# Optimization experiments

Hardware: AMD Instinct MI355X
Metric: run time of the kernel (lower is better)

## Reference

```python
import jax, jax.numpy as jnp
import numpy as np
from jax.scipy.special import logsumexp

N, M, D = 4096, 4096, 512
MASS = 0.9
REG = 0.1
REG_KL = 0.01
ITERS = 100


def setup_inputs() -> dict:
    key = jax.random.key(0)
    k0, k1 = jax.random.split(key)
    return {
        "ft0": jax.random.normal(k0, (N, D), dtype=jnp.float32),
        "ft1": jax.random.normal(k1, (M, D), dtype=jnp.float32),
        "bin_score": jnp.float32(0.4),
    }


def reference(ft0, ft1, bin_score):
    # all rows have norm >> 1e-8 for randn inputs -> foreground masks are all True
    f0 = ft0 / jnp.linalg.norm(ft0, axis=-1, keepdims=True)
    f1 = ft1 / jnp.linalg.norm(ft1, axis=-1, keepdims=True)
    cos_sim = f0 @ f1.T                       # [N, M]
    n, m = cos_sim.shape

    # partial OT marginals with dustbin mass (get_partial_distributions)
    a = jnp.concatenate([jnp.full((n,), MASS / n, jnp.float32),
                         jnp.array([1.0 - MASS], jnp.float32)])
    b = jnp.concatenate([jnp.full((m,), MASS / m, jnp.float32),
                         jnp.array([1.0 - MASS], jnp.float32)])
    log_mu, log_nu = jnp.log(a), jnp.log(b)   # [n+1], [m+1]

    # augment score matrix with dustbin row/col (get_partial_ot_problem)
    top = jnp.concatenate([cos_sim, jnp.broadcast_to(bin_score, (n, 1))], axis=1)
    bot = jnp.broadcast_to(bin_score, (1, m + 1))
    couplings = jnp.concatenate([top, bot], axis=0)   # [n+1, m+1]

    lmba = 1.0 / REG                         # = 10.0
    phi = REG_KL / (REG_KL + 1.0 / lmba)     # = 0.01 / 0.11
    Z = lmba * couplings

    def body(carry, _):
        u, v = carry
        u = (log_mu - logsumexp(Z + v[None, :] * lmba, axis=1)) / lmba * phi
        v = (log_nu - logsumexp(Z + u[:, None] * lmba, axis=0)) / lmba * phi
        return (u, v), None

    u0 = jnp.zeros((n + 1,), jnp.float32)
    v0 = jnp.zeros((m + 1,), jnp.float32)
    (u, v), _ = jax.lax.scan(body, (u0, v0), None, length=ITERS)

    prob = jnp.exp(Z + u[:, None] * lmba + v[None, :] * lmba)
    # prob_add_bkg with all-True masks: identity placement, zero the corner
    return prob.at[-1, -1].set(0.0)
```

## Files before the change

### kernel.cpp

```cpp
#include <hip/hip_runtime.h>
#include <math.h>

#define Nn 4096
#define Mm 4096
#define Dd 512
#define NP 4097
#define NPB 4104

#define PHI 0.09090909090909091f
#define LMU_IN  (-8.4231266823771690f)
#define LMU_BIN (-2.3025850929940457f)
#define LOG_NP  8.3180489582454150f

typedef __attribute__((ext_vector_type(8))) __bf16 bf16x8;
typedef __attribute__((ext_vector_type(4))) float  f32x4;

__device__ __forceinline__ void load_lds16(const __bf16* g, __bf16* l) {
    __builtin_amdgcn_global_load_lds(
        (__attribute__((address_space(1))) void*)g,
        (__attribute__((address_space(3))) void*)l,
        16, 0, 0);
}

__device__ __forceinline__ float block_allreduce_256(float v, float* sb) {
    #pragma unroll
    for (int off = 32; off > 0; off >>= 1) v += __shfl_down(v, off, 64);
    __syncthreads();
    if ((threadIdx.x & 63) == 0) sb[threadIdx.x >> 6] = v;
    __syncthreads();
    return sb[0] + sb[1] + sb[2] + sb[3];
}

__global__ __launch_bounds__(256) void normalize_bins_kernel(
    const float* __restrict__ F0, const float* __restrict__ F1,
    const float* __restrict__ binp,
    __bf16* __restrict__ A, __bf16* __restrict__ B, _Float16* __restrict__ Ef,
    float* __restrict__ S0, float* __restrict__ TcA) {
    __shared__ float sb[4];
    const int row = blockIdx.x;
    const float* src = (row < Nn) ? (F0 + (size_t)row * Dd)
                                  : (F1 + (size_t)(row - Nn) * Dd);
    __bf16* dst = (row < Nn) ? (A + (size_t)row * Dd)
                             : (B + (size_t)(row - Nn) * Dd);
    const float2 x = ((const float2*)src)[threadIdx.x];
    const float s = block_allreduce_256(x.x * x.x + x.y * x.y, sb);
    const float rn = rsqrtf(s);
    dst[2 * threadIdx.x]     = (__bf16)(x.x * rn);
    dst[2 * threadIdx.x + 1] = (__bf16)(x.y * rn);

    if (row < 17) {
        const int j = row * 256 + threadIdx.x;
        if (j < NP) Ef[(size_t)Nn * NPB + j] = (_Float16)__expf(10.0f * binp[0]);
    } else if (row < 33) {
        const int i = (row - 17) * 256 + threadIdx.x;
        Ef[(size_t)i * NPB + Mm] = (_Float16)__expf(10.0f * binp[0]);
    } else if (row < 50) {
        const int k = (row - 33) * 256 + threadIdx.x;
        if (k < NP) S0[k] = 0.f;
    } else if (row < 67) {
        const int k = (row - 50) * 256 + threadIdx.x;
        if (k < NP) TcA[k] = 0.f;
    }
}

#define BKh 32
__global__ __launch_bounds__(512, 2) void gemm_rowsum_kernel(
    const __bf16* __restrict__ A, const __bf16* __restrict__ B,
    _Float16* __restrict__ Ef, float* __restrict__ S0) {
    __shared__ __align__(16) __bf16 As[2][2][256 * BKh];
    __shared__ __align__(16) __bf16 Bs[2][2][256 * BKh];
    const int tid = threadIdx.x;
    const int l = tid & 63, wv = tid >> 6;
    const int wm = wv >> 2, wn = wv & 3;
    const int ln = l & 15, lq = l >> 4;

    const int bid = blockIdx.x;
    const int xcd = bid & 7, sub = bid >> 3;
    const int by = (xcd & 3) * 4 + (sub >> 3);
    const int bx = (xcd >> 2) * 8 + (sub & 7);
    const int row0 = by << 8, col0 = bx << 8;

    f32x4 acc[8][4];
    #pragma unroll
    for (int i = 0; i < 8; ++i)
        #pragma unroll
        for (int j = 0; j < 4; ++j) acc[i][j] = (f32x4){0.f, 0.f, 0.f, 0.f};

    size_t aG[2], bG[2]; int qE[2];
    #pragma unroll
    for (int p = 0; p < 2; ++p) {
        const int q = tid + p * 512;
        const int r = q >> 2, c = q & 3;
        const int cg = c ^ ((r >> 1) & 3);
        aG[p] = (size_t)(row0 + r) * Dd + cg * 8;
        bG[p] = (size_t)(col0 + r) * Dd + cg * 8;
        qE[p] = q * 8;
    }

    auto STAGE_UNIT = [&](int nb, int tt, int u) {
        const size_t kofs = (size_t)(tt * 64 + (u >> 1) * 32);
        if ((u & 1) == 0) {
            load_lds16(A + aG[0] + kofs, &As[nb][u >> 1][qE[0]]);
            load_lds16(A + aG[1] + kofs, &As[nb][u >> 1][qE[1]]);
        } else {
            load_lds16(B + bG[0] + kofs, &Bs[nb][u >> 1][qE[0]]);
            load_lds16(B + bG[1] + kofs, &Bs[nb][u >> 1][qE[1]]);
        }
    };

    #define WAITV(N) asm volatile("s_waitcnt vmcnt(" #N ")" ::: "memory")
    #define BAR() __builtin_amdgcn_s_barrier()

    const int swz2 = (ln >> 1) & 3;

    STAGE_UNIT(0, 0, 0); STAGE_UNIT(0, 0, 1);
    STAGE_UNIT(0, 0, 2); STAGE_UNIT(0, 0, 3);
    WAITV(4); BAR();

    #pragma unroll
    for (int t = 0; t < 8; ++t) {
        const int buf = t & 1, nbuf = buf ^ 1;
        #pragma unroll
        for (int ks = 0; ks < 2; ++ks) {
            bf16x8 bfr[4];
            #pragma unroll
            for (int half = 0; half < 2; ++half) {
                const int p = ks * 2 + half;
                if (half == 0) {
                    #pragma unroll
                    for (int ni = 0; ni < 4; ++ni) {
                        const int r = wn * 64 + ni * 16 + ln;
                        bfr[ni] = *(const bf16x8*)
                            &Bs[buf][ks][r * BKh + ((lq ^ swz2) * 8)];
                    }
                }
                bf16x8 af[4];
                #pragma unroll
                for (int i = 0; i < 4; ++i) {
                    const int r = wm * 128 + half * 64 + i * 16 + ln;
                    af[i] = *(const bf16x8*)
                        &As[buf][ks][r * BKh + ((lq ^ swz2) * 8)];
                }
                if (t < 7) STAGE_UNIT(nbuf, t + 1, p);
                if (t < 7 || p == 0) { WAITV(4); }
                else if (p == 1)     { WAITV(0); }
                BAR();
                __builtin_amdgcn_s_setprio(1);
                #pragma unroll
                for (int i = 0; i < 4; ++i)
                    #pragma unroll
                    for (int ni = 0; ni < 4; ++ni)
                        acc[half * 4 + i][ni] =
                            __builtin_amdgcn_mfma_f32_16x16x32_bf16(
                                af[i], bfr[ni], acc[half * 4 + i][ni], 0, 0, 0);
                __builtin_amdgcn_s_setprio(0);
                BAR();
            }
        }
    }
    #undef WAITV
    #undef BAR

    #pragma unroll
    for (int mi = 0; mi < 8; ++mi) {
        #pragma unroll
        for (int r = 0; r < 4; ++r) {
            const int gi = row0 + wm * 128 + mi * 16 + lq * 4 + r;
            _Float16* bRow = Ef + (size_t)gi * NPB + col0 + wn * 64 + ln;
            float rs = 0.f;
            #pragma unroll
            for (int ni = 0; ni < 4; ++ni) {
                const float e = __expf(10.0f * acc[mi][ni][r]);
                bRow[ni * 16] = (_Float16)e;
                rs += e;
            }
            rs += __shfl_down(rs, 8, 64);
            rs += __shfl_down(rs, 4, 64);
            rs += __shfl_down(rs, 2, 64);
            rs += __shfl_down(rs, 1, 64);
            if (ln == 0) atomicAdd(&S0[gi], rs);
        }
    }
}

__global__ __launch_bounds__(256) void col_pass_kernel(
    const _Float16* __restrict__ Ef, const float* __restrict__ S0,
    const float* __restrict__ eUarr, const float* __restrict__ binp,
    float* __restrict__ Tc, const int mode) {
    __shared__ float evl[32];
    const int tid = threadIdx.x;
    const int t = blockIdx.x;
    const int sI = blockIdx.y;
    const int r0 = sI * 32;

    if (tid < 32) {
        const int r = r0 + tid;
        float ev;
        if (mode == 0) {
            const float ebin = __expf(10.0f * binp[0]);
            ev = __expf(PHI * (LMU_IN - __logf(S0[r] + ebin)));
        } else {
            ev = eUarr[r];
        }
        evl[tid] = ev;
    }
    __syncthreads();

    const int j0 = t * 512 + tid * 2;
    const unsigned short* base = (const unsigned short*)Ef;
    float s0 = 0.f, s1 = 0.f;
    #pragma unroll
    for (int k = 0; k < 32; ++k) {
        const int r = r0 + k;
        union { unsigned u; _Float16 h[2]; } e;
        e.u = *(const unsigned*)(base + (size_t)r * NPB + j0);
        const float ev = evl[k];
        s0 += (float)e.h[0] * ev;
        s1 += (float)e.h[1] * ev;
    }

    float ev4096 = 0.f;
    if (sI == 127) {
        ev4096 = (mode == 0)
               ? __expf(PHI * (LMU_BIN - (LOG_NP + 10.0f * binp[0])))
               : eUarr[Nn];
        union { unsigned u; _Float16 h[2]; } e;
        e.u = *(const unsigned*)(base + (size_t)Nn * NPB + j0);
        s0 += (float)e.h[0] * ev4096;
        s1 += (float)e.h[1] * ev4096;
    }
    atomicAdd(&Tc[j0], s0);
    atomicAdd(&Tc[j0 + 1], s1);

    if (t == 0 && tid < 64) {
        float sc = 0.f;
        if (tid < 32)
            sc = (float)Ef[(size_t)(r0 + tid) * NPB + Mm] * evl[tid];
        else if (tid == 32 && sI == 127)
            sc = (float)Ef[(size_t)Nn * NPB + Mm] * ev4096;
        #pragma unroll
        for (int off = 32; off > 0; off >>= 1) sc += __shfl_down(sc, off, 64);
        if (tid == 0) atomicAdd(&Tc[Mm], sc);
    }
}

__global__ __launch_bounds__(256) void row_pass2_kernel(
    const _Float16* __restrict__ Ef, const float* __restrict__ TcA,
    float* __restrict__ eU, float* __restrict__ TcB) {
    __shared__ float sb[4];
    __shared__ float wl[NP];
    const int tid = threadIdx.x;

    for (int j = tid; j < NP; j += 256) {
        const float lnu = (j < Mm) ? LMU_IN : LMU_BIN;
        wl[j] = __expf(PHI * (lnu - __logf(TcA[j])));
    }
    __syncthreads();

    const int i0 = blockIdx.x * 8;
    #pragma unroll 1
    for (int k = 0; k < 8; ++k) {
        const int i = i0 + k;
        if (i >= NP) break;
        const uint4* rowp = (const uint4*)(Ef + (size_t)i * NPB);
        float s = 0.f;
        #pragma unroll
        for (int c = 0; c < 2; ++c) {
            const int chunk = c * 256 + tid;
            union { uint4 u; _Float16 h[8]; } e;
            e.u = rowp[chunk];
            const float4 w0 = *(const float4*)&wl[chunk * 8];
            const float4 w1 = *(const float4*)&wl[chunk * 8 + 4];
            s += (float)e.h[0] * w0.x + (float)e.h[1] * w0.y
               + (float)e.h[2] * w0.z + (float)e.h[3] * w0.w
               + (float)e.h[4] * w1.x + (float)e.h[5] * w1.y
               + (float)e.h[6] * w1.z + (float)e.h[7] * w1.w;
        }
        if (tid == 0) s += (float)Ef[(size_t)i * NPB + Mm] * wl[Mm];
        s = block_allreduce_256(s, sb);
        if (tid == 0) {
            const float lmu = (i < Nn) ? LMU_IN : LMU_BIN;
            eU[i] = __expf(PHI * (lmu - __logf(s)));
        }
    }
    if (tid < 8 && i0 + tid < NP) TcB[i0 + tid] = 0.f;
}

__global__ __launch_bounds__(256) void finish_kernel(
    const _Float16* __restrict__ Ef, const float* __restrict__ eU,
    const float* __restrict__ TcB, float* __restrict__ out) {
    __shared__ float wl[NP];
    const int tid = threadIdx.x;
    for (int j = tid; j < NP; j += 256) {
        const float lnu = (j < Mm) ? LMU_IN : LMU_BIN;
        wl[j] = __expf(PHI * (lnu - __logf(TcB[j])));
    }
    __syncthreads();

    const int i0 = blockIdx.x * 8;
    #pragma unroll 1
    for (int k = 0; k < 8; ++k) {
        const int i = i0 + k;
        if (i >= NP) break;
        const float sU = eU[i];
        const unsigned* erow32 = (const unsigned*)(Ef + (size_t)i * NPB);
        float* orow = out + (size_t)i * NP;
        #pragma unroll
        for (int c = 0; c < 8; ++c) {
            const int j0 = c * 512 + tid * 2;
            union { unsigned u; _Float16 h[2]; } e;
            e.u = erow32[c * 256 + tid];
            const float2 wv = *(const float2*)&wl[j0];
            orow[j0]     = (float)e.h[0] * sU * wv.x;
            orow[j0 + 1] = (float)e.h[1] * sU * wv.y;
        }
        if (tid == 0) {
            float v = (float)Ef[(size_t)i * NPB + Mm] * sU * wl[Mm];
            if (i == Nn) v = 0.f;
            orow[Mm] = v;
        }
    }
}


extern "C" void kernel_launch(void* const* d_in, const int* in_sizes, int n_in,
                              void* d_out, int out_size, void* d_ws, size_t ws_size,
                              hipStream_t stream) {
    const float* ft0 = (const float*)d_in[0];
    const float* ft1 = (const float*)d_in[1];
    const float* bin = (const float*)d_in[2];
    float* out = (float*)d_out;

    const size_t ABF_B = (size_t)Nn * Dd * 2;
    const size_t EBF_B = (size_t)NP * NPB * 2;
    const size_t VEC_B = 16400;
    __bf16*   Abf = (__bf16*)d_ws;
    __bf16*   Bbf = (__bf16*)((char*)d_ws + ABF_B);
    _Float16* Ef  = (_Float16*)((char*)d_ws + 2 * ABF_B);
    float*    eU  = (float*)((char*)d_ws + 2 * ABF_B + EBF_B);
    float*    S0  = (float*)((char*)d_ws + 2 * ABF_B + EBF_B + VEC_B);
    float*    TcA = (float*)((char*)d_ws + 2 * ABF_B + EBF_B + 2 * VEC_B);
    float*    TcB = (float*)((char*)d_ws + 2 * ABF_B + EBF_B + 3 * VEC_B);

    normalize_bins_kernel<<<Nn + Mm, 256, 0, stream>>>(ft0, ft1, bin,
                                                       Abf, Bbf, Ef, S0, TcA);
    gemm_rowsum_kernel<<<256, 512, 0, stream>>>(Abf, Bbf, Ef, S0);
    col_pass_kernel<<<dim3(8, 128), 256, 0, stream>>>(Ef, S0, eU, bin, TcA, 0);
    row_pass2_kernel<<<513, 256, 0, stream>>>(Ef, TcA, eU, TcB);
    col_pass_kernel<<<dim3(8, 128), 256, 0, stream>>>(Ef, S0, eU, bin, TcB, 1);
    finish_kernel<<<513, 256, 0, stream>>>(Ef, eU, TcB, out);
}
```

Before: 198.1 us.

## Precompute column weight vectors once and enlarge column-pass row chunks

Adds a small kernel that computes the column scaling vector once, so the 513 blocks of the row-pass and finish kernels no longer each recompute 4097 exp/log values and can copy it with vector loads. The column pass now handles 128 rows per block instead of 32, giving a quarter as many float atomics on the column sums. The finish kernel switches to one half-precision element per thread with coalesced per-element stores. This costs two extra kernel launches and less parallelism in the column pass.

```diff
diff --git a/kernel.cpp b/kernel.cpp
--- a/kernel.cpp
+++ b/kernel.cpp
@@ -183,17 +183,28 @@
     }
 }
 
+__global__ __launch_bounds__(256) void wvec_kernel(
+    const float* __restrict__ Tc, float* __restrict__ W,
+    float* __restrict__ Zero) {
+    const int j = blockIdx.x * 256 + threadIdx.x;
+    if (j < NP) {
+        const float lnu = (j < Mm) ? LMU_IN : LMU_BIN;
+        W[j] = __expf(PHI * (lnu - __logf(Tc[j])));
+        if (Zero) Zero[j] = 0.f;
+    }
+}
+
 __global__ __launch_bounds__(256) void col_pass_kernel(
     const _Float16* __restrict__ Ef, const float* __restrict__ S0,
     const float* __restrict__ eUarr, const float* __restrict__ binp,
     float* __restrict__ Tc, const int mode) {
-    __shared__ float evl[32];
+    __shared__ float evl[128];
     const int tid = threadIdx.x;
     const int t = blockIdx.x;
     const int sI = blockIdx.y;
-    const int r0 = sI * 32;
-
-    if (tid < 32) {
+    const int r0 = sI * 128;
+
+    if (tid < 128) {
         const int r = r0 + tid;
         float ev;
         if (mode == 0) {
@@ -209,8 +220,8 @@
     const int j0 = t * 512 + tid * 2;
     const unsigned short* base = (const unsigned short*)Ef;
     float s0 = 0.f, s1 = 0.f;
-    #pragma unroll
-    for (int k = 0; k < 32; ++k) {
+    #pragma unroll 16
+    for (int k = 0; k < 128; ++k) {
         const int r = r0 + k;
         union { unsigned u; _Float16 h[2]; } e;
         e.u = *(const unsigned*)(base + (size_t)r * NPB + j0);
@@ -220,7 +231,7 @@
     }
 
     float ev4096 = 0.f;
-    if (sI == 127) {
+    if (sI == 31) {
         ev4096 = (mode == 0)
                ? __expf(PHI * (LMU_BIN - (LOG_NP + 10.0f * binp[0])))
                : eUarr[Nn];
@@ -232,29 +243,26 @@
     atomicAdd(&Tc[j0], s0);
     atomicAdd(&Tc[j0 + 1], s1);
 
-    if (t == 0 && tid < 64) {
-        float sc = 0.f;
-        if (tid < 32)
-            sc = (float)Ef[(size_t)(r0 + tid) * NPB + Mm] * evl[tid];
-        else if (tid == 32 && sI == 127)
-            sc = (float)Ef[(size_t)Nn * NPB + Mm] * ev4096;
+    if (t == 0 && tid < 128) {
+        float sc = (float)Ef[(size_t)(r0 + tid) * NPB + Mm] * evl[tid];
+        if (sI == 31 && tid == 0)
+            sc += (float)Ef[(size_t)Nn * NPB + Mm] * ev4096;
         #pragma unroll
         for (int off = 32; off > 0; off >>= 1) sc += __shfl_down(sc, off, 64);
-        if (tid == 0) atomicAdd(&Tc[Mm], sc);
+        if ((tid & 63) == 0) atomicAdd(&Tc[Mm], sc);
     }
 }
 
 __global__ __launch_bounds__(256) void row_pass2_kernel(
-    const _Float16* __restrict__ Ef, const float* __restrict__ TcA,
-    float* __restrict__ eU, float* __restrict__ TcB) {
+    const _Float16* __restrict__ Ef, const float* __restrict__ W1,
+    float* __restrict__ eU) {
     __shared__ float sb[4];
     __shared__ float wl[NP];
     const int tid = threadIdx.x;
 
-    for (int j = tid; j < NP; j += 256) {
-        const float lnu = (j < Mm) ? LMU_IN : LMU_BIN;
-        wl[j] = __expf(PHI * (lnu - __logf(TcA[j])));
-    }
+    for (int c = tid; c < 1024; c += 256)
+        ((float4*)wl)[c] = ((const float4*)W1)[c];
+    if (tid == 0) wl[Mm] = W1[Mm];
     __syncthreads();
 
     const int i0 = blockIdx.x * 8;
@@ -283,18 +291,16 @@
             eU[i] = __expf(PHI * (lmu - __logf(s)));
         }
     }
-    if (tid < 8 && i0 + tid < NP) TcB[i0 + tid] = 0.f;
 }
 
 __global__ __launch_bounds__(256) void finish_kernel(
     const _Float16* __restrict__ Ef, const float* __restrict__ eU,
-    const float* __restrict__ TcB, float* __restrict__ out) {
+    const float* __restrict__ W2, float* __restrict__ out) {
     __shared__ float wl[NP];
     const int tid = threadIdx.x;
-    for (int j = tid; j < NP; j += 256) {
-        const float lnu = (j < Mm) ? LMU_IN : LMU_BIN;
-        wl[j] = __expf(PHI * (lnu - __logf(TcB[j])));
-    }
+    for (int c = tid; c < 1024; c += 256)
+        ((float4*)wl)[c] = ((const float4*)W2)[c];
+    if (tid == 0) wl[Mm] = W2[Mm];
     __syncthreads();
 
     const int i0 = blockIdx.x * 8;
@@ -303,16 +309,14 @@
         const int i = i0 + k;
         if (i >= NP) break;
         const float sU = eU[i];
-        const unsigned* erow32 = (const unsigned*)(Ef + (size_t)i * NPB);
+        const unsigned short* erow = (const unsigned short*)(Ef + (size_t)i * NPB);
         float* orow = out + (size_t)i * NP;
         #pragma unroll
-        for (int c = 0; c < 8; ++c) {
-            const int j0 = c * 512 + tid * 2;
-            union { unsigned u; _Float16 h[2]; } e;
-            e.u = erow32[c * 256 + tid];
-            const float2 wv = *(const float2*)&wl[j0];
-            orow[j0]     = (float)e.h[0] * sU * wv.x;
-            orow[j0 + 1] = (float)e.h[1] * sU * wv.y;
+        for (int c = 0; c < 16; ++c) {
+            const int j = c * 256 + tid;
+            union { unsigned short u; _Float16 h; } e;
+            e.u = erow[j];
+            orow[j] = (float)e.h * sU * wl[j];
         }
         if (tid == 0) {
             float v = (float)Ef[(size_t)i * NPB + Mm] * sU * wl[Mm];
@@ -341,12 +345,16 @@
     float*    S0  = (float*)((char*)d_ws + 2 * ABF_B + EBF_B + VEC_B);
     float*    TcA = (float*)((char*)d_ws + 2 * ABF_B + EBF_B + 2 * VEC_B);
     float*    TcB = (float*)((char*)d_ws + 2 * ABF_B + EBF_B + 3 * VEC_B);
+    float*    W1  = (float*)((char*)d_ws + 2 * ABF_B + EBF_B + 4 * VEC_B);
+    float*    W2  = (float*)((char*)d_ws + 2 * ABF_B + EBF_B + 5 * VEC_B);
 
     normalize_bins_kernel<<<Nn + Mm, 256, 0, stream>>>(ft0, ft1, bin,
                                                        Abf, Bbf, Ef, S0, TcA);
     gemm_rowsum_kernel<<<256, 512, 0, stream>>>(Abf, Bbf, Ef, S0);
-    col_pass_kernel<<<dim3(8, 128), 256, 0, stream>>>(Ef, S0, eU, bin, TcA, 0);
-    row_pass2_kernel<<<513, 256, 0, stream>>>(Ef, TcA, eU, TcB);
-    col_pass_kernel<<<dim3(8, 128), 256, 0, stream>>>(Ef, S0, eU, bin, TcB, 1);
-    finish_kernel<<<513, 256, 0, stream>>>(Ef, eU, TcB, out);
-}
+    col_pass_kernel<<<dim3(8, 32), 256, 0, stream>>>(Ef, S0, eU, bin, TcA, 0);
+    wvec_kernel<<<17, 256, 0, stream>>>(TcA, W1, TcB);
+    row_pass2_kernel<<<513, 256, 0, stream>>>(Ef, W1, eU);
+    col_pass_kernel<<<dim3(8, 32), 256, 0, stream>>>(Ef, S0, eU, bin, TcB, 1);
+    wvec_kernel<<<17, 256, 0, stream>>>(TcB, W2, nullptr);
+    finish_kernel<<<513, 256, 0, stream>>>(Ef, eU, W2, out);
+}
```

Measured after the change: 180.8 us. 1.1x faster.
